# Kernel tuning notes

Measured on AMD Instinct MI355X. Metric: run time of the kernel, lower is better.

Reference implementation:

```python
import jax, jax.numpy as jnp
import numpy as np

B, T_OUT, C, L = 8, 8, 64, 1024  # batch, temporal channels, spatial channels (=in_channels), time steps


def setup_inputs() -> dict:
    key = jax.random.key(0)
    ks = jax.random.split(key, 7)
    s = 1.0 / np.sqrt(C)  # conv1d default init scale
    return {
        "x": jax.random.normal(ks[0], (B, T_OUT, C, L), dtype=jnp.float32),
        "Wq": jax.random.uniform(ks[1], (C, C), jnp.float32, -s, s),
        "bq": jax.random.uniform(ks[2], (C,), jnp.float32, -s, s),
        "Wk": jax.random.uniform(ks[3], (C, C), jnp.float32, -s, s),
        "bk": jax.random.uniform(ks[4], (C,), jnp.float32, -s, s),
        "Wv": jax.random.uniform(ks[5], (C, C), jnp.float32, -s, s),
        "bv": jax.random.uniform(ks[6], (C,), jnp.float32, -s, s),
    }


def reference(x, Wq, bq, Wk, bk, Wv, bv):
    b, t, c, l = x.shape
    xr = x.reshape(b * t, c, l)  # [BT, C, L]
    # 1x1 Conv1d == per-timestep linear over channels
    q = jnp.einsum('oc,bcl->bol', Wq, xr) + bq[:, None]
    k = jnp.einsum('oc,bcl->bol', Wk, xr) + bk[:, None]
    v = jnp.einsum('oc,bcl->bol', Wv, xr) + bv[:, None]
    # scores[b, i, j] = sum_c q[b, c, i] * k[b, c, j]  -> [BT, L, L]
    scores = jnp.einsum('bci,bcj->bij', q, k)
    weights = jax.nn.softmax(scores, axis=-1)
    # out[b, i, c] = sum_j weights[b, i, j] * v[b, c, j]
    out = jnp.einsum('bij,bcj->bic', weights, v)
    out = jnp.transpose(out, (0, 2, 1))  # [BT, C, L]
    return out.reshape(b, t, c, l)
```

## Files before the change

### kernel.cpp

```cpp
#include <hip/hip_runtime.h>

#define CC 64
#define LL 1024
#define LOG2E 1.44269504f

typedef unsigned short u16;
typedef unsigned int u32;
typedef __attribute__((ext_vector_type(8))) short short8;
typedef __attribute__((ext_vector_type(4))) float floatx4;

static __device__ __forceinline__ u16 f2b(float f) {
  return (u16)((__float_as_uint(f) + 0x8000u) >> 16);
}
static __device__ __forceinline__ u32 pk2(float a, float b) {
  return ((__float_as_uint(a) + 0x8000u) >> 16) |
         ((__float_as_uint(b) + 0x8000u) & 0xffff0000u);
}
static __device__ __forceinline__ u32 pk2t(float a, float b) {
  return __builtin_amdgcn_perm(__float_as_uint(b), __float_as_uint(a), 0x07060302u);
}
static __device__ __forceinline__ short8 mk8(u32 a, u32 b, u32 c, u32 d) {
  union { u32 u[4]; short8 s; } t;
  t.u[0] = a; t.u[1] = b; t.u[2] = c; t.u[3] = d;
  return t.s;
}

__global__ __launch_bounds__(256) void w_prep(
    const float* __restrict__ Wq, const float* __restrict__ bq,
    const float* __restrict__ Wk, const float* __restrict__ bk,
    const float* __restrict__ Wv, const float* __restrict__ bv,
    u16* __restrict__ whi, float* __restrict__ bsc)
{
  const int idx = blockIdx.x * 256 + threadIdx.x;
  const int m = idx >> 12;
  const float* W = (m == 0) ? Wq : (m == 1) ? Wk : Wv;
  const float w = W[idx & 4095] * ((m == 0) ? LOG2E : 1.0f);
  whi[idx] = f2b(w);
  if (blockIdx.x == 0 && threadIdx.x < 192)
    bsc[threadIdx.x] = (threadIdx.x < 64) ? bq[threadIdx.x] * LOG2E
                     : (threadIdx.x < 128) ? bk[threadIdx.x - 64] : bv[threadIdx.x - 128];
}

__global__ __launch_bounds__(512) void fused_kernel(
    const float* __restrict__ x,
    const u16* __restrict__ whi, const float* __restrict__ bsc,
    float* __restrict__ out)
{
  __shared__ __align__(16) u16 smem[20480];

  const int tid  = threadIdx.x;
  const int wave = tid >> 6;
  const int lane = tid & 63;
  const int l16  = lane & 15;
  const int quad = lane >> 4;

  const int bt  = blockIdx.x & 63;
  const int ih  = blockIdx.x >> 6;
  const int i0w = (ih << 7) + (wave << 4);

  const int jt  = wave & 3;
  const int ot0 = (wave >> 2) << 1;

  const float* xbt = x + (size_t)bt * CC * LL;

  short8 qf0, qf1;
  {
    const float* xq = xbt + i0w + l16;
    float qx[16];
    #pragma unroll
    for (int e = 0; e < 8; ++e) {
      qx[e]     = xq[(size_t)(quad * 8 + e) * LL];
      qx[8 + e] = xq[(size_t)(quad * 8 + 32 + e) * LL];
    }
    const short8 qxh0 = mk8(pk2(qx[0], qx[1]), pk2(qx[2], qx[3]),
                            pk2(qx[4], qx[5]), pk2(qx[6], qx[7]));
    const short8 qxh1 = mk8(pk2(qx[8], qx[9]), pk2(qx[10], qx[11]),
                            pk2(qx[12], qx[13]), pk2(qx[14], qx[15]));
    u16* tb = smem + 9216 + wave * 1152;
    #pragma unroll
    for (int ot = 0; ot < 4; ++ot) {
      const int off = ((ot * 16 + l16) << 6) + quad * 8;
      const short8 ah0 = *(const short8*)(whi + off);
      const short8 ah1 = *(const short8*)(whi + off + 32);
      floatx4 acc = (floatx4){0.f, 0.f, 0.f, 0.f};
      acc = __builtin_amdgcn_mfma_f32_16x16x32_bf16(ah0, qxh0, acc, 0, 0, 0);
      acc = __builtin_amdgcn_mfma_f32_16x16x32_bf16(ah1, qxh1, acc, 0, 0, 0);
      const float4 bb = *(const float4*)(bsc + ot * 16 + quad * 4);
      uint2 pv;
      pv.x = pk2(acc[0] + bb.x, acc[1] + bb.y);
      pv.y = pk2(acc[2] + bb.z, acc[3] + bb.w);
      *(uint2*)(tb + l16 * 72 + ot * 16 + quad * 4) = pv;
    }
    asm volatile("" ::: "memory");
    qf0 = *(const short8*)(tb + l16 * 72 + quad * 8);
    qf1 = *(const short8*)(tb + l16 * 72 + quad * 8 + 32);
    asm volatile("" ::: "memory");
  }

  floatx4 O[4];
  #pragma unroll
  for (int cf = 0; cf < 4; ++cf)
    O[cf] = (floatx4){0.f, 0.f, 0.f, 0.f};
  float lsA = 0.f, lsB = 0.f;

  const int jloc = jt * 16 + l16;
  const int srow = (jloc & 32) | ((jloc & 4) << 2) | ((jloc & 24) >> 1) | (jloc & 3);

  auto proj = [&](const float (&px)[16], u16* Kb, u16* Vb) {
    const short8 xh0 = mk8(pk2(px[0], px[1]), pk2(px[2], px[3]),
                           pk2(px[4], px[5]), pk2(px[6], px[7]));
    const short8 xh1 = mk8(pk2(px[8], px[9]), pk2(px[10], px[11]),
                           pk2(px[12], px[13]), pk2(px[14], px[15]));
    #pragma unroll
    for (int o2 = 0; o2 < 2; ++o2) {
      const int ot = ot0 + o2;
      {
        const int off = 4096 + ((ot * 16 + l16) << 6) + quad * 8;
        const short8 ah0 = *(const short8*)(whi + off);
        const short8 ah1 = *(const short8*)(whi + off + 32);
        floatx4 acc = (floatx4){0.f, 0.f, 0.f, 0.f};
        acc = __builtin_amdgcn_mfma_f32_16x16x32_bf16(ah0, xh0, acc, 0, 0, 0);
        acc = __builtin_amdgcn_mfma_f32_16x16x32_bf16(ah1, xh1, acc, 0, 0, 0);
        const float4 bb = *(const float4*)(bsc + 64 + ot * 16 + quad * 4);
        uint2 pv;
        pv.x = pk2(acc[0] + bb.x, acc[1] + bb.y);
        pv.y = pk2(acc[2] + bb.z, acc[3] + bb.w);
        *(uint2*)(Kb + srow * 72 + ot * 16 + quad * 4) = pv;
      }
      {
        const int off = 8192 + ((ot * 16 + l16) << 6) + quad * 8;
        const short8 ah0 = *(const short8*)(whi + off);
        const short8 ah1 = *(const short8*)(whi + off + 32);
        floatx4 acc = (floatx4){0.f, 0.f, 0.f, 0.f};
        acc = __builtin_amdgcn_mfma_f32_16x16x32_bf16(ah0, xh0, acc, 0, 0, 0);
        acc = __builtin_amdgcn_mfma_f32_16x16x32_bf16(ah1, xh1, acc, 0, 0, 0);
        const float4 bb = *(const float4*)(bsc + 128 + ot * 16 + quad * 4);
        #pragma unroll
        for (int r = 0; r < 4; ++r) {
          const float ov = acc[r] + ((const float*)&bb)[r];
          Vb[(ot * 16 + quad * 4 + r) * 72 + jloc] = f2b(ov);
        }
      }
    }
  };

  {
    float p0[16];
    const float* xp = xbt + jt * 16 + l16;
    #pragma unroll
    for (int e = 0; e < 8; ++e) {
      p0[e]     = xp[(size_t)(quad * 8 + e) * LL];
      p0[8 + e] = xp[(size_t)(quad * 8 + 32 + e) * LL];
    }
    proj(p0, smem, smem + 4608);
  }
  __syncthreads();

  for (int t = 0; t < 16; ++t) {
    const u16* Kc = smem + (t & 1) * 9216;
    const u16* Vc = Kc + 4608;

    float px[16];
    if (t < 15) {
      const float* xp = xbt + ((t + 1) << 6) + jt * 16 + l16;
      #pragma unroll
      for (int e = 0; e < 8; ++e) {
        px[e]     = xp[(size_t)(quad * 8 + e) * LL];
        px[8 + e] = xp[(size_t)(quad * 8 + 32 + e) * LL];
      }
    }

    floatx4 S[4];
    __builtin_amdgcn_s_setprio(1);
    #pragma unroll
    for (int jt2 = 0; jt2 < 4; ++jt2) {
      const u16* ka = Kc + (jt2 * 16 + l16) * 72 + quad * 8;
      const short8 a0 = *(const short8*)(ka);
      const short8 a1 = *(const short8*)(ka + 32);
      floatx4 acc = (floatx4){0.f, 0.f, 0.f, 0.f};
      acc = __builtin_amdgcn_mfma_f32_16x16x32_bf16(a0, qf0, acc, 0, 0, 0);
      acc = __builtin_amdgcn_mfma_f32_16x16x32_bf16(a1, qf1, acc, 0, 0, 0);
      S[jt2] = acc;
    }
    __builtin_amdgcn_s_setprio(0);

    short8 v0f[4], v1f[4];
    #pragma unroll
    for (int cf = 0; cf < 4; ++cf) {
      const u16* va = Vc + (cf * 16 + l16) * 72 + quad * 8;
      v0f[cf] = *(const short8*)(va);
      v1f[cf] = *(const short8*)(va + 32);
    }

    uint2 pp[4];
    #pragma unroll
    for (int jt2 = 0; jt2 < 4; ++jt2) {
      const float e0 = __builtin_amdgcn_exp2f(S[jt2][0]);
      const float e1 = __builtin_amdgcn_exp2f(S[jt2][1]);
      const float e2 = __builtin_amdgcn_exp2f(S[jt2][2]);
      const float e3 = __builtin_amdgcn_exp2f(S[jt2][3]);
      lsA += e0 + e1;
      lsB += e2 + e3;
      pp[jt2].x = pk2t(e0, e1);
      pp[jt2].y = pk2t(e2, e3);
    }

    __builtin_amdgcn_s_setprio(1);
    {
      const short8 pa0 = mk8(pp[0].x, pp[0].y, pp[1].x, pp[1].y);
      const short8 pa1 = mk8(pp[2].x, pp[2].y, pp[3].x, pp[3].y);
      #pragma unroll
      for (int cf = 0; cf < 4; ++cf) {
        O[cf] = __builtin_amdgcn_mfma_f32_16x16x32_bf16(pa0, v0f[cf], O[cf], 0, 0, 0);
        O[cf] = __builtin_amdgcn_mfma_f32_16x16x32_bf16(pa1, v1f[cf], O[cf], 0, 0, 0);
      }
    }
    __builtin_amdgcn_s_setprio(0);

    if (t < 15) {
      u16* Kn = smem + ((t + 1) & 1) * 9216;
      proj(px, Kn, Kn + 4608);
    }
    __syncthreads();
  }

  float lsum = lsA + lsB;
  lsum += __shfl_xor(lsum, 16, 64);
  lsum += __shfl_xor(lsum, 32, 64);

  float* ofw = (float*)smem + wave * 1280;
  #pragma unroll
  for (int r = 0; r < 4; ++r) {
    const float rl = __builtin_amdgcn_rcpf(__shfl(lsum, quad * 4 + r, 64));
    #pragma unroll
    for (int cf = 0; cf < 4; ++cf)
      O[cf][r] *= rl;
  }
  asm volatile("" ::: "memory");
  #pragma unroll
  for (int cf = 0; cf < 4; ++cf)
    #pragma unroll
    for (int r = 0; r < 4; ++r)
      ofw[(cf * 16 + l16) * 20 + quad * 4 + r] = O[cf][r];
  asm volatile("" ::: "memory");
  {
    float* ob = out + (size_t)bt * CC * LL + i0w;
    #pragma unroll
    for (int rr = 0; rr < 4; ++rr) {
      const int c = rr * 16 + l16;
      float4 val = *(const float4*)(ofw + c * 20 + quad * 4);
      *(float4*)(ob + (size_t)c * LL + quad * 4) = val;
    }
  }
  asm volatile("" ::: "memory");
}

extern "C" void kernel_launch(void* const* d_in, const int* in_sizes, int n_in,
                              void* d_out, int out_size, void* d_ws, size_t ws_size,
                              hipStream_t stream) {
  const float* x  = (const float*)d_in[0];
  const float* Wq = (const float*)d_in[1];
  const float* bq = (const float*)d_in[2];
  const float* Wk = (const float*)d_in[3];
  const float* bk = (const float*)d_in[4];
  const float* Wv = (const float*)d_in[5];
  const float* bv = (const float*)d_in[6];
  float* out = (float*)d_out;

  u16* whi = (u16*)d_ws;
  float* bsc = (float*)(whi + 3 * 64 * 64);

  w_prep<<<48, 256, 0, stream>>>(Wq, bq, Wk, bk, Wv, bv, whi, bsc);
  fused_kernel<<<512, 512, 0, stream>>>(x, whi, bsc, out);
}
```

Before: 129.1 us.

## Pre-convert x to transposed bf16 in prep kernel and vectorize loads

Adds a prep pass that converts x to bf16 in an [L, C] transposed layout, stored in workspace. The main kernel can then load 16-byte vectors of channels instead of 16 strided fp32 loads per thread, and it no longer repacks them to bf16 inside the loop. The V projection is also reorganised with swapped MFMA operands so it writes packed uint2 stores instead of scattered 16-bit stores, and the bf16 packing uses a perm instruction. In exchange there is an extra full pass over x (read fp32, write bf16) in a larger prep kernel, and more workspace is used.

```diff
diff --git a/kernel.cpp b/kernel.cpp
--- a/kernel.cpp
+++ b/kernel.cpp
@@ -12,9 +12,9 @@
 static __device__ __forceinline__ u16 f2b(float f) {
   return (u16)((__float_as_uint(f) + 0x8000u) >> 16);
 }
-static __device__ __forceinline__ u32 pk2(float a, float b) {
-  return ((__float_as_uint(a) + 0x8000u) >> 16) |
-         ((__float_as_uint(b) + 0x8000u) & 0xffff0000u);
+static __device__ __forceinline__ u32 pk2r(float a, float b) {
+  return __builtin_amdgcn_perm(__float_as_uint(b) + 0x8000u,
+                               __float_as_uint(a) + 0x8000u, 0x07060302u);
 }
 static __device__ __forceinline__ u32 pk2t(float a, float b) {
   return __builtin_amdgcn_perm(__float_as_uint(b), __float_as_uint(a), 0x07060302u);
@@ -25,24 +25,51 @@
   return t.s;
 }
 
-__global__ __launch_bounds__(256) void w_prep(
+__global__ __launch_bounds__(256) void xw_prep(
+    const float* __restrict__ x,
     const float* __restrict__ Wq, const float* __restrict__ bq,
     const float* __restrict__ Wk, const float* __restrict__ bk,
     const float* __restrict__ Wv, const float* __restrict__ bv,
-    u16* __restrict__ whi, float* __restrict__ bsc)
+    u16* __restrict__ xhT, u16* __restrict__ whi, float* __restrict__ bsc)
 {
-  const int idx = blockIdx.x * 256 + threadIdx.x;
-  const int m = idx >> 12;
-  const float* W = (m == 0) ? Wq : (m == 1) ? Wk : Wv;
-  const float w = W[idx & 4095] * ((m == 0) ? LOG2E : 1.0f);
-  whi[idx] = f2b(w);
-  if (blockIdx.x == 0 && threadIdx.x < 192)
-    bsc[threadIdx.x] = (threadIdx.x < 64) ? bq[threadIdx.x] * LOG2E
-                     : (threadIdx.x < 128) ? bk[threadIdx.x - 64] : bv[threadIdx.x - 128];
+  __shared__ __align__(16) u16 xh_s[64 * 72];
+  const int tid = threadIdx.x;
+  const int blk = blockIdx.x;
+  const int bt  = blk & 63;
+  const int l0  = (blk >> 6) << 6;
+
+  if (tid < 12) {
+    const int widx = blk * 12 + tid;
+    const int m = widx >> 12;
+    const float* W = (m == 0) ? Wq : (m == 1) ? Wk : Wv;
+    whi[widx] = f2b(W[widx & 4095] * ((m == 0) ? LOG2E : 1.0f));
+  }
+  if (blk == 0 && tid < 192)
+    bsc[tid] = (tid < 64) ? bq[tid] * LOG2E
+             : (tid < 128) ? bk[tid - 64] : bv[tid - 128];
+
+  const int lx = tid & 63;
+  const int cg = (tid >> 6) << 4;
+  const float* xp = x + ((size_t)bt * CC + cg) * LL + l0 + lx;
+  float v0[16];
+  #pragma unroll
+  for (int e = 0; e < 16; ++e) v0[e] = xp[(size_t)e * LL];
+  #pragma unroll
+  for (int e = 0; e < 16; e += 2)
+    *(u32*)(xh_s + lx * 72 + cg + e) = pk2r(v0[e], v0[e + 1]);
+  __syncthreads();
+
+  const int r_st = tid >> 2;
+  const int c_st = (tid & 3) << 4;
+  u16* gd = xhT + ((size_t)(bt * LL + l0 + r_st)) * CC + c_st;
+  uint4 a = *(const uint4*)(xh_s + r_st * 72 + c_st);
+  uint4 b = *(const uint4*)(xh_s + r_st * 72 + c_st + 8);
+  *(uint4*)(gd) = a;
+  *(uint4*)(gd + 8) = b;
 }
 
 __global__ __launch_bounds__(512) void fused_kernel(
-    const float* __restrict__ x,
+    const u16* __restrict__ xhT,
     const u16* __restrict__ whi, const float* __restrict__ bsc,
     float* __restrict__ out)
 {
@@ -61,21 +88,13 @@
   const int jt  = wave & 3;
   const int ot0 = (wave >> 2) << 1;
 
-  const float* xbt = x + (size_t)bt * CC * LL;
+  const u16* xbt = xhT + (size_t)bt * LL * CC;
 
   short8 qf0, qf1;
   {
-    const float* xq = xbt + i0w + l16;
-    float qx[16];
-    #pragma unroll
-    for (int e = 0; e < 8; ++e) {
-      qx[e]     = xq[(size_t)(quad * 8 + e) * LL];
-      qx[8 + e] = xq[(size_t)(quad * 8 + 32 + e) * LL];
-    }
-    const short8 qxh0 = mk8(pk2(qx[0], qx[1]), pk2(qx[2], qx[3]),
-                            pk2(qx[4], qx[5]), pk2(qx[6], qx[7]));
-    const short8 qxh1 = mk8(pk2(qx[8], qx[9]), pk2(qx[10], qx[11]),
-                            pk2(qx[12], qx[13]), pk2(qx[14], qx[15]));
+    const u16* xq = xbt + (size_t)(i0w + l16) * CC + quad * 8;
+    const short8 qxh0 = *(const short8*)(xq);
+    const short8 qxh1 = *(const short8*)(xq + 32);
     u16* tb = smem + 9216 + wave * 1152;
     #pragma unroll
     for (int ot = 0; ot < 4; ++ot) {
@@ -87,8 +106,8 @@
       acc = __builtin_amdgcn_mfma_f32_16x16x32_bf16(ah1, qxh1, acc, 0, 0, 0);
       const float4 bb = *(const float4*)(bsc + ot * 16 + quad * 4);
       uint2 pv;
-      pv.x = pk2(acc[0] + bb.x, acc[1] + bb.y);
-      pv.y = pk2(acc[2] + bb.z, acc[3] + bb.w);
+      pv.x = pk2r(acc[0] + bb.x, acc[1] + bb.y);
+      pv.y = pk2r(acc[2] + bb.z, acc[3] + bb.w);
       *(uint2*)(tb + l16 * 72 + ot * 16 + quad * 4) = pv;
     }
     asm volatile("" ::: "memory");
@@ -105,54 +124,47 @@
 
   const int jloc = jt * 16 + l16;
   const int srow = (jloc & 32) | ((jloc & 4) << 2) | ((jloc & 24) >> 1) | (jloc & 3);
-
-  auto proj = [&](const float (&px)[16], u16* Kb, u16* Vb) {
-    const short8 xh0 = mk8(pk2(px[0], px[1]), pk2(px[2], px[3]),
-                           pk2(px[4], px[5]), pk2(px[6], px[7]));
-    const short8 xh1 = mk8(pk2(px[8], px[9]), pk2(px[10], px[11]),
-                           pk2(px[12], px[13]), pk2(px[14], px[15]));
+  const float bvv = bsc[128 + ot0 * 16 + l16];
+  const float bvv1 = bsc[128 + (ot0 + 1) * 16 + l16];
+
+  auto proj = [&](short8 xh0, short8 xh1, u16* Kb, u16* Vb) {
     #pragma unroll
     for (int o2 = 0; o2 < 2; ++o2) {
       const int ot = ot0 + o2;
+      const int offK = 4096 + ((ot * 16 + l16) << 6) + quad * 8;
+      const int offV = 8192 + ((ot * 16 + l16) << 6) + quad * 8;
       {
-        const int off = 4096 + ((ot * 16 + l16) << 6) + quad * 8;
-        const short8 ah0 = *(const short8*)(whi + off);
-        const short8 ah1 = *(const short8*)(whi + off + 32);
+        const short8 ah0 = *(const short8*)(whi + offK);
+        const short8 ah1 = *(const short8*)(whi + offK + 32);
         floatx4 acc = (floatx4){0.f, 0.f, 0.f, 0.f};
         acc = __builtin_amdgcn_mfma_f32_16x16x32_bf16(ah0, xh0, acc, 0, 0, 0);
         acc = __builtin_amdgcn_mfma_f32_16x16x32_bf16(ah1, xh1, acc, 0, 0, 0);
         const float4 bb = *(const float4*)(bsc + 64 + ot * 16 + quad * 4);
         uint2 pv;
-        pv.x = pk2(acc[0] + bb.x, acc[1] + bb.y);
-        pv.y = pk2(acc[2] + bb.z, acc[3] + bb.w);
+        pv.x = pk2r(acc[0] + bb.x, acc[1] + bb.y);
+        pv.y = pk2r(acc[2] + bb.z, acc[3] + bb.w);
         *(uint2*)(Kb + srow * 72 + ot * 16 + quad * 4) = pv;
       }
       {
-        const int off = 8192 + ((ot * 16 + l16) << 6) + quad * 8;
-        const short8 ah0 = *(const short8*)(whi + off);
-        const short8 ah1 = *(const short8*)(whi + off + 32);
+        const short8 av0 = *(const short8*)(whi + offV);
+        const short8 av1 = *(const short8*)(whi + offV + 32);
         floatx4 acc = (floatx4){0.f, 0.f, 0.f, 0.f};
-        acc = __builtin_amdgcn_mfma_f32_16x16x32_bf16(ah0, xh0, acc, 0, 0, 0);
-        acc = __builtin_amdgcn_mfma_f32_16x16x32_bf16(ah1, xh1, acc, 0, 0, 0);
-        const float4 bb = *(const float4*)(bsc + 128 + ot * 16 + quad * 4);
-        #pragma unroll
-        for (int r = 0; r < 4; ++r) {
-          const float ov = acc[r] + ((const float*)&bb)[r];
-          Vb[(ot * 16 + quad * 4 + r) * 72 + jloc] = f2b(ov);
-        }
+        acc = __builtin_amdgcn_mfma_f32_16x16x32_bf16(xh0, av0, acc, 0, 0, 0);
+        acc = __builtin_amdgcn_mfma_f32_16x16x32_bf16(xh1, av1, acc, 0, 0, 0);
+        const float bv = o2 ? bvv1 : bvv;
+        uint2 pv;
+        pv.x = pk2r(acc[0] + bv, acc[1] + bv);
+        pv.y = pk2r(acc[2] + bv, acc[3] + bv);
+        *(uint2*)(Vb + (ot * 16 + l16) * 72 + jt * 16 + quad * 4) = pv;
       }
     }
   };
 
   {
-    float p0[16];
-    const float* xp = xbt + jt * 16 + l16;
-    #pragma unroll
-    for (int e = 0; e < 8; ++e) {
-      p0[e]     = xp[(size_t)(quad * 8 + e) * LL];
-      p0[8 + e] = xp[(size_t)(quad * 8 + 32 + e) * LL];
-    }
-    proj(p0, smem, smem + 4608);
+    const u16* xp = xbt + (size_t)jloc * CC + quad * 8;
+    const short8 x0 = *(const short8*)(xp);
+    const short8 x1 = *(const short8*)(xp + 32);
+    proj(x0, x1, smem, smem + 4608);
   }
   __syncthreads();
 
@@ -160,14 +172,11 @@
     const u16* Kc = smem + (t & 1) * 9216;
     const u16* Vc = Kc + 4608;
 
-    float px[16];
+    short8 pxh0, pxh1;
     if (t < 15) {
-      const float* xp = xbt + ((t + 1) << 6) + jt * 16 + l16;
-      #pragma unroll
-      for (int e = 0; e < 8; ++e) {
-        px[e]     = xp[(size_t)(quad * 8 + e) * LL];
-        px[8 + e] = xp[(size_t)(quad * 8 + 32 + e) * LL];
-      }
+      const u16* xp = xbt + (size_t)(((t + 1) << 6) + jloc) * CC + quad * 8;
+      pxh0 = *(const short8*)(xp);
+      pxh1 = *(const short8*)(xp + 32);
     }
 
     floatx4 S[4];
@@ -219,7 +228,7 @@
 
     if (t < 15) {
       u16* Kn = smem + ((t + 1) & 1) * 9216;
-      proj(px, Kn, Kn + 4608);
+      proj(pxh0, pxh1, Kn, Kn + 4608);
     }
     __syncthreads();
   }
@@ -267,9 +276,10 @@
   const float* bv = (const float*)d_in[6];
   float* out = (float*)d_out;
 
-  u16* whi = (u16*)d_ws;
+  u16* xhT = (u16*)d_ws;
+  u16* whi = xhT + (size_t)64 * LL * CC;
   float* bsc = (float*)(whi + 3 * 64 * 64);
 
-  w_prep<<<48, 256, 0, stream>>>(Wq, bq, Wk, bk, Wv, bv, whi, bsc);
-  fused_kernel<<<512, 512, 0, stream>>>(x, whi, bsc, out);
-}
+  xw_prep<<<1024, 256, 0, stream>>>(x, Wq, bq, Wk, bk, Wv, bv, xhT, whi, bsc);
+  fused_kernel<<<512, 512, 0, stream>>>(xhT, whi, bsc, out);
+}
```

New measurement: 123.1 us. 1.05x faster.
